# Performance work log

Hardware: AMD Instinct MI355X
Metric: run time of the kernel (lower is better)

Reference implementation:

```python
import jax, jax.numpy as jnp
import numpy as np

EMBED_DIM = 512
NUM_HEADS = 8
HEAD_DIM = EMBED_DIM // NUM_HEADS


def setup_inputs() -> dict:
    key = jax.random.key(0)
    ks = jax.random.split(key, 6)
    B, S, E = 2, 4096, EMBED_DIM
    scale = 1.0 / np.sqrt(E)
    return {
        "rotation_params": jax.random.normal(ks[0], (E, E), jnp.float32) * scale,
        "entangle_params": jax.random.normal(ks[1], (E, E), jnp.float32) * scale,
        "inputs": jax.random.normal(ks[2], (B, S, E), jnp.float32),
        "w_q": jax.random.normal(ks[3], (E, E), jnp.float32) * scale,
        "w_k": jax.random.normal(ks[4], (E, E), jnp.float32) * scale,
        "w_v": jax.random.normal(ks[5], (E, E), jnp.float32) * scale,
    }


def reference(rotation_params, entangle_params, inputs, w_q, w_k, w_v):
    B, S, E = inputs.shape
    H, D = NUM_HEADS, HEAD_DIM
    # torch nn.Linear(x) = x @ W.T ; then extra matmul with rotation/entangle mats
    q = (inputs @ w_q.T) @ rotation_params  # [B,S,E]
    k = (inputs @ w_k.T) @ entangle_params  # [B,S,E]
    v = inputs @ w_v.T                       # [B,S,E]
    # split heads -> [B,H,S,D]
    q = q.reshape(B, S, H, D).transpose(0, 2, 1, 3)
    k = k.reshape(B, S, H, D).transpose(0, 2, 1, 3)
    v = v.reshape(B, S, H, D).transpose(0, 2, 1, 3)
    scores = jnp.einsum("bhqd,bhkd->bhqk", q, k) / jnp.sqrt(jnp.float32(D))
    attn = jax.nn.softmax(scores, axis=-1)  # dropout p=0 (eval) -> identity
    out = jnp.einsum("bhqk,bhkd->bhqd", attn, v)
    return out.transpose(0, 2, 1, 3).reshape(B, S, E)
```

## Files before the change

### kernel.cpp

```cpp
#include <hip/hip_runtime.h>
#include <cstddef>

#define E 512
#define H 8
#define D 64
#define BATCH 2
#define SEQ 4096

typedef __attribute__((ext_vector_type(8))) short bf16x8;
typedef __attribute__((ext_vector_type(4))) float f32x4;
typedef __attribute__((ext_vector_type(16))) float f32x16;
typedef __attribute__((ext_vector_type(4))) unsigned uint4v;

__device__ __forceinline__ ushort f2bf(float f) {
  unsigned u = __builtin_bit_cast(unsigned, f);
  u += 0x7fff + ((u >> 16) & 1);
  return (ushort)(u >> 16);
}
__device__ __forceinline__ float bf2f(ushort h) {
  return __builtin_bit_cast(float, (unsigned)h << 16);
}
__device__ __forceinline__ unsigned pk_bf16(float lo, float hi) {
#if __has_builtin(__builtin_amdgcn_cvt_pk_bf16_f32)
  typedef __attribute__((ext_vector_type(2))) __bf16 bfv2;
  bfv2 r = __builtin_amdgcn_cvt_pk_bf16_f32(lo, hi);
  return __builtin_bit_cast(unsigned, r);
#else
  return (unsigned)f2bf(lo) | ((unsigned)f2bf(hi) << 16);
#endif
}
__device__ __forceinline__ float fexp2(float x) {
#if __has_builtin(__builtin_amdgcn_exp2f)
  return __builtin_amdgcn_exp2f(x);
#else
  return exp2f(x);
#endif
}
__device__ __forceinline__ void permswap32(unsigned& a, unsigned& b) {
  asm volatile("v_permlane32_swap_b32 %0, %1" : "+v"(a), "+v"(b));
}

__global__ __launch_bounds__(256) void xcast(const float* __restrict__ x,
                                             ushort* __restrict__ xh,
                                             ushort* __restrict__ xl) {
  size_t i = ((size_t)blockIdx.x * 256 + threadIdx.x) * 4;
  float4 v = *(const float4*)&x[i];
  ushort4 h, l;
  h.x = f2bf(v.x); l.x = f2bf(v.x - bf2f(h.x));
  h.y = f2bf(v.y); l.y = f2bf(v.y - bf2f(h.y));
  h.z = f2bf(v.z); l.z = f2bf(v.z - bf2f(h.z));
  h.w = f2bf(v.w); l.w = f2bf(v.w - bf2f(h.w));
  *(ushort4*)&xh[i] = h;
  *(ushort4*)&xl[i] = l;
}

__global__ __launch_bounds__(256) void fold_tiled(
    const float* __restrict__ wq, const float* __restrict__ wk,
    const float* __restrict__ rot, const float* __restrict__ ent,
    ushort* __restrict__ weffbT) {
  const int which = blockIdx.z;
  const float* w = which ? wk : wq;
  const float* r = which ? ent : rot;
  const int k = blockIdx.x * 256 + threadIdx.x;
  const int n0 = blockIdx.y * 8;
  float acc[8] = {};
  for (int j0 = 0; j0 < E; j0 += 16) {
    float wv_[16];
#pragma unroll
    for (int u = 0; u < 16; ++u) wv_[u] = w[(size_t)(j0 + u) * E + k];
#pragma unroll
    for (int u = 0; u < 16; ++u)
#pragma unroll
      for (int t = 0; t < 8; ++t)
        acc[t] += wv_[u] * r[(size_t)(j0 + u) * E + n0 + t];
  }
#pragma unroll
  for (int t = 0; t < 8; ++t)
    weffbT[(size_t)which * E * E + (size_t)(n0 + t) * E + k] = f2bf(acc[t]);
}

__global__ __launch_bounds__(256) void wv_cast(const float* __restrict__ wv,
                                               ushort* __restrict__ dst) {
  size_t i = ((size_t)blockIdx.x * 256 + threadIdx.x) * 4;
  float4 v = *(const float4*)&wv[i];
  ushort4 o;
  o.x = f2bf(v.x); o.y = f2bf(v.y); o.z = f2bf(v.z); o.w = f2bf(v.w);
  *(ushort4*)&dst[i] = o;
}

#define LDA 40

__global__ __launch_bounds__(256) void qkv_fused(
    const ushort* __restrict__ xhg, const ushort* __restrict__ xlg,
    const ushort* __restrict__ weffbT, ushort* __restrict__ qg,
    ushort* __restrict__ kg, ushort* __restrict__ vtg) {
  __shared__ ushort sm[5 * 64 * LDA];
  ushort* Ah = sm;
  ushort* Al = sm + 64 * LDA;
  ushort* Bs = sm + 2 * 64 * LDA;
  ushort* vt_tile = Bs;

  const int head = blockIdx.x;
  const int m0 = blockIdx.y * 64;
  const int tid = threadIdx.x;
  const int wave = tid >> 6, lane = tid & 63;
  const int l15 = lane & 15, quad = lane >> 4;
  const int ar = tid >> 2, ac8 = (tid & 3) * 8;

  const ushort* arow = xhg + (size_t)(m0 + ar) * E + ac8;
  const ushort* lrow = xlg + (size_t)(m0 + ar) * E + ac8;
  const ushort* b0row = weffbT + (size_t)(head * 64 + ar) * E + ac8;

  f32x4 acc[3][4];
#pragma unroll
  for (int w = 0; w < 3; ++w)
#pragma unroll
    for (int nt = 0; nt < 4; ++nt) acc[w][nt] = (f32x4){0.f, 0.f, 0.f, 0.f};

  uint4 pa_h = *(const uint4*)&arow[0];
  uint4 pa_l = *(const uint4*)&lrow[0];
  uint4 pb0 = *(const uint4*)&b0row[0];
  uint4 pb1 = *(const uint4*)&b0row[E * E];
  uint4 pb2 = *(const uint4*)&b0row[2 * E * E];

  for (int k0 = 0; k0 < E; k0 += 32) {
    __syncthreads();
    *(uint4*)&Ah[ar * LDA + ac8] = pa_h;
    *(uint4*)&Al[ar * LDA + ac8] = pa_l;
    *(uint4*)&Bs[0 * 64 * LDA + ar * LDA + ac8] = pb0;
    *(uint4*)&Bs[1 * 64 * LDA + ar * LDA + ac8] = pb1;
    *(uint4*)&Bs[2 * 64 * LDA + ar * LDA + ac8] = pb2;
    __syncthreads();

    const int kn = (k0 + 32 < E) ? k0 + 32 : 0;
    pa_h = *(const uint4*)&arow[kn];
    pa_l = *(const uint4*)&lrow[kn];
    pb0 = *(const uint4*)&b0row[kn];
    pb1 = *(const uint4*)&b0row[E * E + kn];
    pb2 = *(const uint4*)&b0row[2 * E * E + kn];

    bf16x8 ah = *(const bf16x8*)&Ah[(wave * 16 + l15) * LDA + quad * 8];
    bf16x8 al = *(const bf16x8*)&Al[(wave * 16 + l15) * LDA + quad * 8];
#pragma unroll
    for (int w = 0; w < 3; ++w)
#pragma unroll
      for (int nt = 0; nt < 4; ++nt) {
        bf16x8 bf = *(const bf16x8*)&Bs[w * 64 * LDA + (nt * 16 + l15) * LDA +
                                        quad * 8];
        acc[w][nt] =
            __builtin_amdgcn_mfma_f32_16x16x32_bf16(ah, bf, acc[w][nt], 0, 0, 0);
        acc[w][nt] =
            __builtin_amdgcn_mfma_f32_16x16x32_bf16(al, bf, acc[w][nt], 0, 0, 0);
      }
  }

  const int b = m0 >> 12;
  const int s_base = m0 & (SEQ - 1);
  const float QSCALE = 0.125f * 1.44269504f;

#pragma unroll
  for (int w = 0; w < 2; ++w) {
    ushort* dst = (w == 0) ? qg : kg;
    float sc = (w == 0) ? QSCALE : 1.0f;
#pragma unroll
    for (int nt = 0; nt < 4; ++nt)
#pragma unroll
      for (int r = 0; r < 4; ++r) {
        float v = acc[w][nt][r] * sc;
        float vo = __shfl_xor(v, 1);
        if (!(lane & 1)) {
          int s = s_base + wave * 16 + quad * 4 + r;
          size_t ix = ((size_t)(b * H + head) * SEQ + s) * D + nt * 16 + l15;
          *(unsigned*)&dst[ix] = pk_bf16(v, vo);
        }
      }
  }

  __syncthreads();
#pragma unroll
  for (int nt = 0; nt < 4; ++nt) {
    uint2 w2;
    w2.x = pk_bf16(acc[2][nt][0], acc[2][nt][1]);
    w2.y = pk_bf16(acc[2][nt][2], acc[2][nt][3]);
    *(uint2*)&vt_tile[(nt * 16 + l15) * 72 + wave * 16 + quad * 4] = w2;
  }
  __syncthreads();
  {
    int vr = tid >> 2, vs = (tid & 3) * 16;
    uint4 c0 = *(const uint4*)&vt_tile[vr * 72 + vs];
    uint4 c1 = *(const uint4*)&vt_tile[vr * 72 + vs + 8];
    size_t vo = ((size_t)(b * H + head) * D + vr) * SEQ + s_base + vs;
    *(uint4*)&vtg[vo] = c0;
    *(uint4*)&vtg[vo + 8] = c1;
  }
}

#define LDK 72

__global__ __launch_bounds__(512, 3) void attn_mfma(
    const ushort* __restrict__ qg, const ushort* __restrict__ kg,
    const ushort* __restrict__ vtg, float* __restrict__ out) {
  __shared__ ushort sm[4 * 64 * LDK + 256];
  ushort* Ks0 = sm;
  ushort* Vs0 = sm + 2 * 64 * LDK;
  float* lex = (float*)(sm + 4 * 64 * LDK);

  const int qt = blockIdx.x;
  const int bh = blockIdx.y;
  const int tid = threadIdx.x;
  const int wave = tid >> 6;
  const int grp = wave >> 2, wq = wave & 3;
  const int lane = tid & 63;
  const int l31 = lane & 31, hi = lane >> 5;
  const int gtid = tid & 255;

  const ushort* qp = qg + (size_t)bh * SEQ * D;
  const ushort* kp = kg + (size_t)bh * SEQ * D;
  const ushort* vp = vtg + (size_t)bh * D * SEQ;
  ushort* Ksg = Ks0 + grp * 64 * LDK;
  ushort* Vsg = Vs0 + grp * 64 * LDK;

  const int qrow0 = qt * 128 + wq * 32;
  bf16x8 qf[4];
#pragma unroll
  for (int ds = 0; ds < 4; ++ds)
    qf[ds] =
        *(const bf16x8*)&qp[(size_t)(qrow0 + l31) * D + ds * 16 + hi * 8];

  f32x16 o[2];
  o[0] = 0.f;
  o[1] = 0.f;
  float l_r = 0.f;

  const int r0 = gtid >> 3, c0 = (gtid & 7) * 8;
  const int r1 = 32 + r0;

  uint4 pk0 = *(const uint4*)&kp[(size_t)grp * 64 * D + r0 * 64 + c0];
  uint4 pk1 = *(const uint4*)&kp[(size_t)grp * 64 * D + r1 * 64 + c0];
  uint4 pv0 = *(const uint4*)&vp[(size_t)r0 * SEQ + grp * 64 + c0];
  uint4 pv1 = *(const uint4*)&vp[(size_t)r1 * SEQ + grp * 64 + c0];

  for (int it = 0; it < SEQ / 128; ++it) {
    __syncthreads();
    *(uint4*)&Ksg[r0 * LDK + c0] = pk0;
    *(uint4*)&Ksg[r1 * LDK + c0] = pk1;
    *(uint4*)&Vsg[r0 * LDK + c0] = pv0;
    *(uint4*)&Vsg[r1 * LDK + c0] = pv1;
    __syncthreads();

    {
      const int itn = (it + 1 < SEQ / 128) ? it + 1 : it;
      const int ktn = itn * 2 + grp;
      const ushort* ksrc = kp + (size_t)ktn * 64 * D;
      pk0 = *(const uint4*)&ksrc[r0 * 64 + c0];
      pk1 = *(const uint4*)&ksrc[r1 * 64 + c0];
      pv0 = *(const uint4*)&vp[(size_t)r0 * SEQ + ktn * 64 + c0];
      pv1 = *(const uint4*)&vp[(size_t)r1 * SEQ + ktn * 64 + c0];
    }

#pragma unroll
    for (int t = 0; t < 2; ++t) {
      f32x16 st = 0.f;
      __builtin_amdgcn_s_setprio(1);
#pragma unroll
      for (int ds = 0; ds < 4; ++ds) {
        bf16x8 kf =
            *(const bf16x8*)&Ksg[(t * 32 + l31) * LDK + ds * 16 + hi * 8];
        st = __builtin_amdgcn_mfma_f32_32x32x16_bf16(kf, qf[ds], st, 0, 0, 0);
      }
      __builtin_amdgcn_s_setprio(0);

      float pv[16];
#pragma unroll
      for (int r = 0; r < 16; ++r) pv[r] = fexp2(st[r]);
      {
        float s01 = (pv[0] + pv[1]) + (pv[2] + pv[3]);
        float s23 = (pv[4] + pv[5]) + (pv[6] + pv[7]);
        float s45 = (pv[8] + pv[9]) + (pv[10] + pv[11]);
        float s67 = (pv[12] + pv[13]) + (pv[14] + pv[15]);
        l_r += (s01 + s23) + (s45 + s67);
      }

      unsigned w0[4], w1[4];
#pragma unroll
      for (int j = 0; j < 2; ++j) {
        {
          unsigned c0w = pk_bf16(pv[2 * j + 0], pv[2 * j + 1]);
          unsigned c1w = pk_bf16(pv[2 * j + 4], pv[2 * j + 5]);
          permswap32(c0w, c1w);
          w0[j] = c0w;
          w0[2 + j] = c1w;
        }
        {
          unsigned c0w = pk_bf16(pv[2 * j + 8], pv[2 * j + 9]);
          unsigned c1w = pk_bf16(pv[2 * j + 12], pv[2 * j + 13]);
          permswap32(c0w, c1w);
          w1[j] = c0w;
          w1[2 + j] = c1w;
        }
      }
      bf16x8 pf0 =
          __builtin_bit_cast(bf16x8, (uint4v){w0[0], w0[1], w0[2], w0[3]});
      bf16x8 pf1 =
          __builtin_bit_cast(bf16x8, (uint4v){w1[0], w1[1], w1[2], w1[3]});

      __builtin_amdgcn_s_setprio(1);
#pragma unroll
      for (int nt = 0; nt < 2; ++nt) {
        bf16x8 vf0 =
            *(const bf16x8*)&Vsg[(nt * 32 + l31) * LDK + t * 32 + hi * 8];
        o[nt] = __builtin_amdgcn_mfma_f32_32x32x16_bf16(pf0, vf0, o[nt], 0, 0,
                                                        0);
        bf16x8 vf1 = *(const bf16x8*)&Vsg[(nt * 32 + l31) * LDK + t * 32 + 16 +
                                          hi * 8];
        o[nt] = __builtin_amdgcn_mfma_f32_32x32x16_bf16(pf1, vf1, o[nt], 0, 0,
                                                        0);
      }
      __builtin_amdgcn_s_setprio(0);
    }
  }

  __syncthreads();
  float lg = l_r + __shfl_xor(l_r, 32);
  float* Oex = (float*)sm;
  if (grp == 1) {
#pragma unroll
    for (int nt = 0; nt < 2; ++nt)
#pragma unroll
      for (int r = 0; r < 16; ++r) {
        int row = (r & 3) + 8 * (r >> 2) + 4 * hi;
        Oex[(wq * 32 + row) * 68 + nt * 32 + l31] = o[nt][r];
      }
    if (lane < 32) lex[wq * 32 + l31] = lg;
  }
  __syncthreads();
  if (grp == 0) {
    float linv = 1.f / (lg + lex[wq * 32 + l31]);
    const int b = bh >> 3, h = bh & 7;
#pragma unroll
    for (int r = 0; r < 16; ++r) {
      int row = (r & 3) + 8 * (r >> 2) + 4 * hi;
      float inv = __shfl(linv, row);
      int srow = qt * 128 + wq * 32 + row;
#pragma unroll
      for (int nt = 0; nt < 2; ++nt) {
        float val = o[nt][r] + Oex[(wq * 32 + row) * 68 + nt * 32 + l31];
        out[((size_t)b * SEQ + srow) * E + h * D + nt * 32 + l31] = val * inv;
      }
    }
  }
}

extern "C" void kernel_launch(void* const* d_in, const int* in_sizes, int n_in,
                              void* d_out, int out_size, void* d_ws,
                              size_t ws_size, hipStream_t stream) {
  const float* rot = (const float*)d_in[0];
  const float* ent = (const float*)d_in[1];
  const float* x = (const float*)d_in[2];
  const float* wq = (const float*)d_in[3];
  const float* wk = (const float*)d_in[4];
  const float* wv = (const float*)d_in[5];
  float* out = (float*)d_out;

  const size_t NX = (size_t)BATCH * SEQ * E;
  ushort* weffbT = (ushort*)d_ws;
  ushort* xh = weffbT + 3 * E * E;
  ushort* xl = xh + NX;
  ushort* qg = xl + NX;
  ushort* kg = qg + NX;
  ushort* vtg = kg + NX;

  xcast<<<dim3(NX / 1024), 256, 0, stream>>>(x, xh, xl);
  fold_tiled<<<dim3(E / 256, E / 8, 2), 256, 0, stream>>>(wq, wk, rot, ent,
                                                          weffbT);
  wv_cast<<<dim3(E * E / 1024), 256, 0, stream>>>(wv, weffbT + 2 * E * E);
  qkv_fused<<<dim3(H, BATCH * SEQ / 64), 256, 0, stream>>>(xh, xl, weffbT, qg,
                                                           kg, vtg);
  attn_mfma<<<dim3(SEQ / 128, BATCH * H), 512, 0, stream>>>(qg, kg, vtg, out);
}
```

Baseline: 246.6 us.

## Halve attention block waves, give each wave two 32-row query tiles

The attention kernel drops from 8 waves to 4 per block. Each wave now handles 64 query rows as two 32-row sub-tiles, so every K and V fragment read from LDS feeds two MFMAs instead of one. The aim is to cut LDS read traffic per FLOP and give each wave more independent MFMA work. In exchange, register pressure roughly doubles (two sets of Q fragments, S tiles and O accumulators), occupancy bounds drop to 256 threads x 2 blocks, and each thread issues twice as many global loads for the K/V staging.

```diff
diff --git a/kernel.cpp b/kernel.cpp
--- a/kernel.cpp
+++ b/kernel.cpp
@@ -197,7 +197,7 @@
 
 #define LDK 72
 
-__global__ __launch_bounds__(512, 3) void attn_mfma(
+__global__ __launch_bounds__(256, 2) void attn_mfma(
     const ushort* __restrict__ qg, const ushort* __restrict__ kg,
     const ushort* __restrict__ vtg, float* __restrict__ out) {
   __shared__ ushort sm[4 * 64 * LDK + 256];
@@ -209,10 +209,10 @@
   const int bh = blockIdx.y;
   const int tid = threadIdx.x;
   const int wave = tid >> 6;
-  const int grp = wave >> 2, wq = wave & 3;
+  const int grp = wave >> 1, wq = wave & 1;
   const int lane = tid & 63;
   const int l31 = lane & 31, hi = lane >> 5;
-  const int gtid = tid & 255;
+  const int gtid = tid & 127;
 
   const ushort* qp = qg + (size_t)bh * SEQ * D;
   const ushort* kp = kg + (size_t)bh * SEQ * D;
@@ -220,132 +220,165 @@
   ushort* Ksg = Ks0 + grp * 64 * LDK;
   ushort* Vsg = Vs0 + grp * 64 * LDK;
 
-  const int qrow0 = qt * 128 + wq * 32;
-  bf16x8 qf[4];
-#pragma unroll
-  for (int ds = 0; ds < 4; ++ds)
-    qf[ds] =
-        *(const bf16x8*)&qp[(size_t)(qrow0 + l31) * D + ds * 16 + hi * 8];
-
-  f32x16 o[2];
-  o[0] = 0.f;
-  o[1] = 0.f;
-  float l_r = 0.f;
+  const int qrow0 = qt * 128 + wq * 64;
+  bf16x8 qf[2][4];
+#pragma unroll
+  for (int sub = 0; sub < 2; ++sub)
+#pragma unroll
+    for (int ds = 0; ds < 4; ++ds)
+      qf[sub][ds] = *(const bf16x8*)&qp[(size_t)(qrow0 + sub * 32 + l31) * D +
+                                        ds * 16 + hi * 8];
+
+  f32x16 o[2][2];
+#pragma unroll
+  for (int sub = 0; sub < 2; ++sub) {
+    o[sub][0] = 0.f;
+    o[sub][1] = 0.f;
+  }
+  float l_r[2] = {0.f, 0.f};
 
   const int r0 = gtid >> 3, c0 = (gtid & 7) * 8;
-  const int r1 = 32 + r0;
-
-  uint4 pk0 = *(const uint4*)&kp[(size_t)grp * 64 * D + r0 * 64 + c0];
-  uint4 pk1 = *(const uint4*)&kp[(size_t)grp * 64 * D + r1 * 64 + c0];
-  uint4 pv0 = *(const uint4*)&vp[(size_t)r0 * SEQ + grp * 64 + c0];
-  uint4 pv1 = *(const uint4*)&vp[(size_t)r1 * SEQ + grp * 64 + c0];
+
+  uint4 pk[4], pvv4[4];
+#pragma unroll
+  for (int u = 0; u < 4; ++u) {
+    pk[u] = *(const uint4*)&kp[(size_t)(grp * 64 + r0 + u * 16) * D + c0];
+    pvv4[u] = *(const uint4*)&vp[(size_t)(r0 + u * 16) * SEQ + grp * 64 + c0];
+  }
 
   for (int it = 0; it < SEQ / 128; ++it) {
     __syncthreads();
-    *(uint4*)&Ksg[r0 * LDK + c0] = pk0;
-    *(uint4*)&Ksg[r1 * LDK + c0] = pk1;
-    *(uint4*)&Vsg[r0 * LDK + c0] = pv0;
-    *(uint4*)&Vsg[r1 * LDK + c0] = pv1;
+#pragma unroll
+    for (int u = 0; u < 4; ++u) {
+      *(uint4*)&Ksg[(r0 + u * 16) * LDK + c0] = pk[u];
+      *(uint4*)&Vsg[(r0 + u * 16) * LDK + c0] = pvv4[u];
+    }
     __syncthreads();
 
     {
       const int itn = (it + 1 < SEQ / 128) ? it + 1 : it;
       const int ktn = itn * 2 + grp;
-      const ushort* ksrc = kp + (size_t)ktn * 64 * D;
-      pk0 = *(const uint4*)&ksrc[r0 * 64 + c0];
-      pk1 = *(const uint4*)&ksrc[r1 * 64 + c0];
-      pv0 = *(const uint4*)&vp[(size_t)r0 * SEQ + ktn * 64 + c0];
-      pv1 = *(const uint4*)&vp[(size_t)r1 * SEQ + ktn * 64 + c0];
+#pragma unroll
+      for (int u = 0; u < 4; ++u) {
+        pk[u] =
+            *(const uint4*)&kp[(size_t)(ktn * 64 + r0 + u * 16) * D + c0];
+        pvv4[u] =
+            *(const uint4*)&vp[(size_t)(r0 + u * 16) * SEQ + ktn * 64 + c0];
+      }
     }
 
 #pragma unroll
     for (int t = 0; t < 2; ++t) {
-      f32x16 st = 0.f;
+      f32x16 st[2];
+      st[0] = 0.f;
+      st[1] = 0.f;
       __builtin_amdgcn_s_setprio(1);
 #pragma unroll
       for (int ds = 0; ds < 4; ++ds) {
         bf16x8 kf =
             *(const bf16x8*)&Ksg[(t * 32 + l31) * LDK + ds * 16 + hi * 8];
-        st = __builtin_amdgcn_mfma_f32_32x32x16_bf16(kf, qf[ds], st, 0, 0, 0);
+        st[0] =
+            __builtin_amdgcn_mfma_f32_32x32x16_bf16(kf, qf[0][ds], st[0], 0, 0, 0);
+        st[1] =
+            __builtin_amdgcn_mfma_f32_32x32x16_bf16(kf, qf[1][ds], st[1], 0, 0, 0);
       }
       __builtin_amdgcn_s_setprio(0);
 
-      float pv[16];
-#pragma unroll
-      for (int r = 0; r < 16; ++r) pv[r] = fexp2(st[r]);
-      {
-        float s01 = (pv[0] + pv[1]) + (pv[2] + pv[3]);
-        float s23 = (pv[4] + pv[5]) + (pv[6] + pv[7]);
-        float s45 = (pv[8] + pv[9]) + (pv[10] + pv[11]);
-        float s67 = (pv[12] + pv[13]) + (pv[14] + pv[15]);
-        l_r += (s01 + s23) + (s45 + s67);
-      }
-
-      unsigned w0[4], w1[4];
-#pragma unroll
-      for (int j = 0; j < 2; ++j) {
+      bf16x8 pfA[2], pfB[2];
+#pragma unroll
+      for (int sub = 0; sub < 2; ++sub) {
+        float pv[16];
+#pragma unroll
+        for (int r = 0; r < 16; ++r) pv[r] = fexp2(st[sub][r]);
         {
-          unsigned c0w = pk_bf16(pv[2 * j + 0], pv[2 * j + 1]);
-          unsigned c1w = pk_bf16(pv[2 * j + 4], pv[2 * j + 5]);
-          permswap32(c0w, c1w);
-          w0[j] = c0w;
-          w0[2 + j] = c1w;
+          float s01 = (pv[0] + pv[1]) + (pv[2] + pv[3]);
+          float s23 = (pv[4] + pv[5]) + (pv[6] + pv[7]);
+          float s45 = (pv[8] + pv[9]) + (pv[10] + pv[11]);
+          float s67 = (pv[12] + pv[13]) + (pv[14] + pv[15]);
+          l_r[sub] += (s01 + s23) + (s45 + s67);
         }
-        {
-          unsigned c0w = pk_bf16(pv[2 * j + 8], pv[2 * j + 9]);
-          unsigned c1w = pk_bf16(pv[2 * j + 12], pv[2 * j + 13]);
-          permswap32(c0w, c1w);
-          w1[j] = c0w;
-          w1[2 + j] = c1w;
+        unsigned w0[4], w1[4];
+#pragma unroll
+        for (int j = 0; j < 2; ++j) {
+          {
+            unsigned c0w = pk_bf16(pv[2 * j + 0], pv[2 * j + 1]);
+            unsigned c1w = pk_bf16(pv[2 * j + 4], pv[2 * j + 5]);
+            permswap32(c0w, c1w);
+            w0[j] = c0w;
+            w0[2 + j] = c1w;
+          }
+          {
+            unsigned c0w = pk_bf16(pv[2 * j + 8], pv[2 * j + 9]);
+            unsigned c1w = pk_bf16(pv[2 * j + 12], pv[2 * j + 13]);
+            permswap32(c0w, c1w);
+            w1[j] = c0w;
+            w1[2 + j] = c1w;
+          }
         }
-      }
-      bf16x8 pf0 =
-          __builtin_bit_cast(bf16x8, (uint4v){w0[0], w0[1], w0[2], w0[3]});
-      bf16x8 pf1 =
-          __builtin_bit_cast(bf16x8, (uint4v){w1[0], w1[1], w1[2], w1[3]});
+        pfA[sub] =
+            __builtin_bit_cast(bf16x8, (uint4v){w0[0], w0[1], w0[2], w0[3]});
+        pfB[sub] =
+            __builtin_bit_cast(bf16x8, (uint4v){w1[0], w1[1], w1[2], w1[3]});
+      }
 
       __builtin_amdgcn_s_setprio(1);
 #pragma unroll
       for (int nt = 0; nt < 2; ++nt) {
         bf16x8 vf0 =
             *(const bf16x8*)&Vsg[(nt * 32 + l31) * LDK + t * 32 + hi * 8];
-        o[nt] = __builtin_amdgcn_mfma_f32_32x32x16_bf16(pf0, vf0, o[nt], 0, 0,
-                                                        0);
         bf16x8 vf1 = *(const bf16x8*)&Vsg[(nt * 32 + l31) * LDK + t * 32 + 16 +
                                           hi * 8];
-        o[nt] = __builtin_amdgcn_mfma_f32_32x32x16_bf16(pf1, vf1, o[nt], 0, 0,
-                                                        0);
+        o[0][nt] = __builtin_amdgcn_mfma_f32_32x32x16_bf16(pfA[0], vf0,
+                                                           o[0][nt], 0, 0, 0);
+        o[0][nt] = __builtin_amdgcn_mfma_f32_32x32x16_bf16(pfB[0], vf1,
+                                                           o[0][nt], 0, 0, 0);
+        o[1][nt] = __builtin_amdgcn_mfma_f32_32x32x16_bf16(pfA[1], vf0,
+                                                           o[1][nt], 0, 0, 0);
+        o[1][nt] = __builtin_amdgcn_mfma_f32_32x32x16_bf16(pfB[1], vf1,
+                                                           o[1][nt], 0, 0, 0);
       }
       __builtin_amdgcn_s_setprio(0);
     }
   }
 
   __syncthreads();
-  float lg = l_r + __shfl_xor(l_r, 32);
+  float lg[2];
+#pragma unroll
+  for (int sub = 0; sub < 2; ++sub)
+    lg[sub] = l_r[sub] + __shfl_xor(l_r[sub], 32);
   float* Oex = (float*)sm;
   if (grp == 1) {
 #pragma unroll
-    for (int nt = 0; nt < 2; ++nt)
+    for (int sub = 0; sub < 2; ++sub)
+#pragma unroll
+      for (int nt = 0; nt < 2; ++nt)
+#pragma unroll
+        for (int r = 0; r < 16; ++r) {
+          int row = (r & 3) + 8 * (r >> 2) + 4 * hi;
+          Oex[(wq * 64 + sub * 32 + row) * 68 + nt * 32 + l31] = o[sub][nt][r];
+        }
+    if (lane < 32) {
+      lex[wq * 64 + l31] = lg[0];
+      lex[wq * 64 + 32 + l31] = lg[1];
+    }
+  }
+  __syncthreads();
+  if (grp == 0) {
+    const int b = bh >> 3, h = bh & 7;
+#pragma unroll
+    for (int sub = 0; sub < 2; ++sub) {
+      float linv = 1.f / (lg[sub] + lex[wq * 64 + sub * 32 + l31]);
 #pragma unroll
       for (int r = 0; r < 16; ++r) {
         int row = (r & 3) + 8 * (r >> 2) + 4 * hi;
-        Oex[(wq * 32 + row) * 68 + nt * 32 + l31] = o[nt][r];
-      }
-    if (lane < 32) lex[wq * 32 + l31] = lg;
-  }
-  __syncthreads();
-  if (grp == 0) {
-    float linv = 1.f / (lg + lex[wq * 32 + l31]);
-    const int b = bh >> 3, h = bh & 7;
-#pragma unroll
-    for (int r = 0; r < 16; ++r) {
-      int row = (r & 3) + 8 * (r >> 2) + 4 * hi;
-      float inv = __shfl(linv, row);
-      int srow = qt * 128 + wq * 32 + row;
-#pragma unroll
-      for (int nt = 0; nt < 2; ++nt) {
-        float val = o[nt][r] + Oex[(wq * 32 + row) * 68 + nt * 32 + l31];
-        out[((size_t)b * SEQ + srow) * E + h * D + nt * 32 + l31] = val * inv;
+        float inv = __shfl(linv, row);
+        int srow = qt * 128 + wq * 64 + sub * 32 + row;
+#pragma unroll
+        for (int nt = 0; nt < 2; ++nt) {
+          float val =
+              o[sub][nt][r] + Oex[(wq * 64 + sub * 32 + row) * 68 + nt * 32 + l31];
+          out[((size_t)b * SEQ + srow) * E + h * D + nt * 32 + l31] = val * inv;
+        }
       }
     }
   }
@@ -376,5 +409,5 @@
   wv_cast<<<dim3(E * E / 1024), 256, 0, stream>>>(wv, weffbT + 2 * E * E);
   qkv_fused<<<dim3(H, BATCH * SEQ / 64), 256, 0, stream>>>(xh, xl, weffbT, qg,
                                                            kg, vtg);
-  attn_mfma<<<dim3(SEQ / 128, BATCH * H), 512, 0, stream>>>(qg, kg, vtg, out);
-}
+  attn_mfma<<<dim3(SEQ / 128, BATCH * H), 256, 0, stream>>>(qg, kg, vtg, out);
+}
```

New measurement: 331.3 us. 1.34x slower.

## Drop split-KV wave groups in attention kernel, use 256-thread blocks

Applied to the files above, without the earlier changes.

The attention kernel no longer splits each block's key range across two 4-wave groups that merge partial outputs through shared memory at the end. Each block now runs 4 waves over all 64 KV tiles serially, with half the shared memory and launch bounds of 256 threads at 4 blocks per CU. This removes the end-of-kernel reduction and its extra barriers, but doubles the serial loop length per block and halves the waves per block, so latency hiding now rests on occupancy.

```diff
diff --git a/kernel.cpp b/kernel.cpp
--- a/kernel.cpp
+++ b/kernel.cpp
@@ -197,30 +197,24 @@
 
 #define LDK 72
 
-__global__ __launch_bounds__(512, 3) void attn_mfma(
+__global__ __launch_bounds__(256, 4) void attn_mfma(
     const ushort* __restrict__ qg, const ushort* __restrict__ kg,
     const ushort* __restrict__ vtg, float* __restrict__ out) {
-  __shared__ ushort sm[4 * 64 * LDK + 256];
-  ushort* Ks0 = sm;
-  ushort* Vs0 = sm + 2 * 64 * LDK;
-  float* lex = (float*)(sm + 4 * 64 * LDK);
+  __shared__ ushort Ks[64 * LDK];
+  __shared__ ushort Vs[64 * LDK];
 
   const int qt = blockIdx.x;
   const int bh = blockIdx.y;
   const int tid = threadIdx.x;
   const int wave = tid >> 6;
-  const int grp = wave >> 2, wq = wave & 3;
   const int lane = tid & 63;
   const int l31 = lane & 31, hi = lane >> 5;
-  const int gtid = tid & 255;
 
   const ushort* qp = qg + (size_t)bh * SEQ * D;
   const ushort* kp = kg + (size_t)bh * SEQ * D;
   const ushort* vp = vtg + (size_t)bh * D * SEQ;
-  ushort* Ksg = Ks0 + grp * 64 * LDK;
-  ushort* Vsg = Vs0 + grp * 64 * LDK;
-
-  const int qrow0 = qt * 128 + wq * 32;
+
+  const int qrow0 = qt * 128 + wave * 32;
   bf16x8 qf[4];
 #pragma unroll
   for (int ds = 0; ds < 4; ++ds)
@@ -232,30 +226,29 @@
   o[1] = 0.f;
   float l_r = 0.f;
 
-  const int r0 = gtid >> 3, c0 = (gtid & 7) * 8;
+  const int r0 = tid >> 3, c0 = (tid & 7) * 8;
   const int r1 = 32 + r0;
 
-  uint4 pk0 = *(const uint4*)&kp[(size_t)grp * 64 * D + r0 * 64 + c0];
-  uint4 pk1 = *(const uint4*)&kp[(size_t)grp * 64 * D + r1 * 64 + c0];
-  uint4 pv0 = *(const uint4*)&vp[(size_t)r0 * SEQ + grp * 64 + c0];
-  uint4 pv1 = *(const uint4*)&vp[(size_t)r1 * SEQ + grp * 64 + c0];
-
-  for (int it = 0; it < SEQ / 128; ++it) {
+  uint4 pk0 = *(const uint4*)&kp[(size_t)r0 * D + c0];
+  uint4 pk1 = *(const uint4*)&kp[(size_t)r1 * D + c0];
+  uint4 pv0 = *(const uint4*)&vp[(size_t)r0 * SEQ + c0];
+  uint4 pv1 = *(const uint4*)&vp[(size_t)r1 * SEQ + c0];
+
+  for (int it = 0; it < SEQ / 64; ++it) {
     __syncthreads();
-    *(uint4*)&Ksg[r0 * LDK + c0] = pk0;
-    *(uint4*)&Ksg[r1 * LDK + c0] = pk1;
-    *(uint4*)&Vsg[r0 * LDK + c0] = pv0;
-    *(uint4*)&Vsg[r1 * LDK + c0] = pv1;
+    *(uint4*)&Ks[r0 * LDK + c0] = pk0;
+    *(uint4*)&Ks[r1 * LDK + c0] = pk1;
+    *(uint4*)&Vs[r0 * LDK + c0] = pv0;
+    *(uint4*)&Vs[r1 * LDK + c0] = pv1;
     __syncthreads();
 
     {
-      const int itn = (it + 1 < SEQ / 128) ? it + 1 : it;
-      const int ktn = itn * 2 + grp;
-      const ushort* ksrc = kp + (size_t)ktn * 64 * D;
-      pk0 = *(const uint4*)&ksrc[r0 * 64 + c0];
-      pk1 = *(const uint4*)&ksrc[r1 * 64 + c0];
-      pv0 = *(const uint4*)&vp[(size_t)r0 * SEQ + ktn * 64 + c0];
-      pv1 = *(const uint4*)&vp[(size_t)r1 * SEQ + ktn * 64 + c0];
+      const int itn = (it + 1 < SEQ / 64) ? it + 1 : it;
+      const ushort* ksrc = kp + (size_t)itn * 64 * D;
+      pk0 = *(const uint4*)&ksrc[r0 * D + c0];
+      pk1 = *(const uint4*)&ksrc[r1 * D + c0];
+      pv0 = *(const uint4*)&vp[(size_t)r0 * SEQ + itn * 64 + c0];
+      pv1 = *(const uint4*)&vp[(size_t)r1 * SEQ + itn * 64 + c0];
     }
 
 #pragma unroll
@@ -265,7 +258,7 @@
 #pragma unroll
       for (int ds = 0; ds < 4; ++ds) {
         bf16x8 kf =
-            *(const bf16x8*)&Ksg[(t * 32 + l31) * LDK + ds * 16 + hi * 8];
+            *(const bf16x8*)&Ks[(t * 32 + l31) * LDK + ds * 16 + hi * 8];
         st = __builtin_amdgcn_mfma_f32_32x32x16_bf16(kf, qf[ds], st, 0, 0, 0);
       }
       __builtin_amdgcn_s_setprio(0);
@@ -308,11 +301,11 @@
 #pragma unroll
       for (int nt = 0; nt < 2; ++nt) {
         bf16x8 vf0 =
-            *(const bf16x8*)&Vsg[(nt * 32 + l31) * LDK + t * 32 + hi * 8];
+            *(const bf16x8*)&Vs[(nt * 32 + l31) * LDK + t * 32 + hi * 8];
         o[nt] = __builtin_amdgcn_mfma_f32_32x32x16_bf16(pf0, vf0, o[nt], 0, 0,
                                                         0);
-        bf16x8 vf1 = *(const bf16x8*)&Vsg[(nt * 32 + l31) * LDK + t * 32 + 16 +
-                                          hi * 8];
+        bf16x8 vf1 = *(const bf16x8*)&Vs[(nt * 32 + l31) * LDK + t * 32 + 16 +
+                                         hi * 8];
         o[nt] = __builtin_amdgcn_mfma_f32_32x32x16_bf16(pf1, vf1, o[nt], 0, 0,
                                                         0);
       }
@@ -320,33 +313,18 @@
     }
   }
 
-  __syncthreads();
   float lg = l_r + __shfl_xor(l_r, 32);
-  float* Oex = (float*)sm;
-  if (grp == 1) {
-#pragma unroll
-    for (int nt = 0; nt < 2; ++nt)
-#pragma unroll
-      for (int r = 0; r < 16; ++r) {
-        int row = (r & 3) + 8 * (r >> 2) + 4 * hi;
-        Oex[(wq * 32 + row) * 68 + nt * 32 + l31] = o[nt][r];
-      }
-    if (lane < 32) lex[wq * 32 + l31] = lg;
-  }
-  __syncthreads();
-  if (grp == 0) {
-    float linv = 1.f / (lg + lex[wq * 32 + l31]);
-    const int b = bh >> 3, h = bh & 7;
-#pragma unroll
-    for (int r = 0; r < 16; ++r) {
-      int row = (r & 3) + 8 * (r >> 2) + 4 * hi;
-      float inv = __shfl(linv, row);
-      int srow = qt * 128 + wq * 32 + row;
-#pragma unroll
-      for (int nt = 0; nt < 2; ++nt) {
-        float val = o[nt][r] + Oex[(wq * 32 + row) * 68 + nt * 32 + l31];
-        out[((size_t)b * SEQ + srow) * E + h * D + nt * 32 + l31] = val * inv;
-      }
+  float linv = 1.f / lg;
+  const int b = bh >> 3, h = bh & 7;
+#pragma unroll
+  for (int r = 0; r < 16; ++r) {
+    int row = (r & 3) + 8 * (r >> 2) + 4 * hi;
+    float inv = __shfl(linv, row);
+    int srow = qt * 128 + wave * 32 + row;
+#pragma unroll
+    for (int nt = 0; nt < 2; ++nt) {
+      out[((size_t)b * SEQ + srow) * E + h * D + nt * 32 + l31] =
+          o[nt][r] * inv;
     }
   }
 }
@@ -376,5 +354,5 @@
   wv_cast<<<dim3(E * E / 1024), 256, 0, stream>>>(wv, weffbT + 2 * E * E);
   qkv_fused<<<dim3(H, BATCH * SEQ / 64), 256, 0, stream>>>(xh, xl, weffbT, qg,
                                                            kg, vtg);
-  attn_mfma<<<dim3(SEQ / 128, BATCH * H), 512, 0, stream>>>(qg, kg, vtg, out);
-}
+  attn_mfma<<<dim3(SEQ / 128, BATCH * H), 256, 0, stream>>>(qg, kg, vtg, out);
+}
```

Result: slower. 251.6 us (+2.0%).
